# Kernel optimization log

Measured on AMD Instinct MI355X. Metric: run time of the kernel, lower is better.

The kernel has to match this reference:

```python
import jax, jax.numpy as jnp
import numpy as np

B, N, K, D, OUT = 4, 65536, 16, 8, 8
EPS = 1e-6      # BatchNorm eps from module
SLOPE = 0.2     # LeakyReLU negative slope


def setup_inputs() -> dict:
    key = jax.random.key(0)
    ks = jax.random.split(key, 4)
    coords = jax.random.normal(ks[0], (B, N, 3), jnp.float32)
    features = jax.random.normal(ks[1], (B, D, N, 1), jnp.float32)
    neighbour_indices = jax.random.randint(ks[2], (B, N, K), 0, N)
    conv_w = jax.random.normal(ks[3], (OUT, 10), jnp.float32) * 0.1  # 1x1 Conv2d weight (out,in)
    conv_b = jnp.zeros((OUT,), jnp.float32)
    bn_gamma = jnp.ones((OUT,), jnp.float32)
    bn_beta = jnp.zeros((OUT,), jnp.float32)
    return dict(coords=coords, features=features, neighbour_indices=neighbour_indices,
                conv_w=conv_w, conv_b=conv_b, bn_gamma=bn_gamma, bn_beta=bn_beta)


def _locse(coords, features, neighbour_indices, conv_w, conv_b, bn_gamma, bn_beta):
    # per-batch gather: (B,N,d),(B,N,K) -> (B,N,K,d)
    gather = jax.vmap(lambda x, i: x[i])
    nb_coords = gather(coords, neighbour_indices)                      # (B,N,K,3)
    ext = jnp.broadcast_to(coords[:, :, None, :], nb_coords.shape)     # (B,N,K,3)
    rel_pos = ext - nb_coords
    rel_dist = jnp.sqrt(jnp.sum(rel_pos * rel_pos, -1, keepdims=True))  # (B,N,K,1)
    rf = jnp.concatenate([rel_dist, rel_pos, ext, nb_coords], -1)       # (B,N,K,10)
    # SharedMLP: 1x1 conv + BatchNorm (training stats, biased var) + LeakyReLU(0.2)
    y = jnp.einsum('bnkc,oc->bnko', rf, conv_w) + conv_b                # (B,N,K,OUT)
    mean = jnp.mean(y, (0, 1, 2))
    var = jnp.mean(jnp.square(y - mean), (0, 1, 2))
    y = bn_gamma * (y - mean) * jax.lax.rsqrt(var + EPS) + bn_beta
    y = jnp.where(y >= 0, y, SLOPE * y)
    # neighbour feature gather: features (B,D,N,1) -> (B,N,D) -> (B,N,K,D)
    nf = gather(jnp.squeeze(features, -1).transpose(0, 2, 1), neighbour_indices)
    out = jnp.concatenate([nf, y], -1)                                  # (B,N,K,D+OUT)
    # match torch channel-first layout (B, 2*d, N, K)
    return jnp.moveaxis(out, -1, 1), jnp.moveaxis(y, -1, 1)


def reference(coords, features, neighbour_indices, conv_w, conv_b, bn_gamma, bn_beta):
    return _locse(coords, features, neighbour_indices, conv_w, conv_b, bn_gamma, bn_beta)
```

## Files before the change

kernel.cpp:

```cpp
#include <hip/hip_runtime.h>
#include <cstdint>
#include <cstddef>

namespace {
constexpr int Bn = 4;
constexpr int Nn = 65536;
constexpr int Kn = 16;
constexpr int NK = Nn * Kn;
constexpr int TOTAL = Bn * NK;
constexpr float COUNT_F = 4194304.0f;
constexpr float EPS = 1e-6f;
constexpr float SLOPE = 0.2f;
constexpr long long OUT0_TOTAL = (long long)Bn * 16 * NK;
}


__global__ __launch_bounds__(256) void prep_kernel(
    const float* __restrict__ coords,
    const float* __restrict__ features,
    float* __restrict__ stats,
    float4* __restrict__ cpad,
    float4* __restrict__ tf)
{
    if (blockIdx.x == 0 && threadIdx.x < 16) stats[threadIdx.x] = 0.0f;
    int t = blockIdx.x * blockDim.x + threadIdx.x;
    if (t >= Bn * Nn) return;
    int b = t >> 16;
    int n = t & (Nn - 1);
    const float* c = coords + (size_t)t * 3;
    cpad[t] = make_float4(c[0], c[1], c[2], 0.0f);
    const float* fb = features + (size_t)b * 8 * Nn + n;
    float4 lo = make_float4(fb[0 * Nn], fb[1 * Nn], fb[2 * Nn], fb[3 * Nn]);
    float4 hi = make_float4(fb[4 * Nn], fb[5 * Nn], fb[6 * Nn], fb[7 * Nn]);
    tf[2 * t]     = lo;
    tf[2 * t + 1] = hi;
}

__global__ void init_kernel(float* __restrict__ stats) {
    if (threadIdx.x < 16) stats[threadIdx.x] = 0.0f;
}

template <bool PREP>
__global__ __launch_bounds__(256) void reduce_kernel(
    const int* __restrict__ nbr,
    const float4* __restrict__ cpad,
    const float* __restrict__ coords,
    const float* __restrict__ conv_w,
    const float* __restrict__ conv_b,
    float* __restrict__ stats)
{
    float w[80];
    #pragma unroll
    for (int i = 0; i < 80; i++) w[i] = conv_w[i];
    float bb[8];
    #pragma unroll
    for (int i = 0; i < 8; i++) bb[i] = conv_b[i];

    float s[8], sq[8];
    #pragma unroll
    for (int i = 0; i < 8; i++) { s[i] = 0.0f; sq[i] = 0.0f; }

    int stride = gridDim.x * blockDim.x;
    for (int t = blockIdx.x * blockDim.x + threadIdx.x; t < TOTAL; t += stride) {
        int b = t >> 20;
        int r = t & (NK - 1);
        int n = r >> 4;
        int idx = nbr[t];
        float ex, ey, ez, nx, ny, nz;
        if (PREP) {
            float4 e = cpad[(b << 16) + n];
            float4 q = cpad[(b << 16) + idx];
            ex = e.x; ey = e.y; ez = e.z;
            nx = q.x; ny = q.y; nz = q.z;
        } else {
            const float* cb = coords + (size_t)b * Nn * 3;
            ex = cb[n * 3]; ey = cb[n * 3 + 1]; ez = cb[n * 3 + 2];
            nx = cb[idx * 3]; ny = cb[idx * 3 + 1]; nz = cb[idx * 3 + 2];
        }
        float rx = ex - nx, ry = ey - ny, rz = ez - nz;
        float dist = sqrtf(rx * rx + ry * ry + rz * rz);
        float rf[10] = {dist, rx, ry, rz, ex, ey, ez, nx, ny, nz};
        #pragma unroll
        for (int o = 0; o < 8; o++) {
            float y = bb[o];
            #pragma unroll
            for (int c = 0; c < 10; c++) y = fmaf(w[o * 10 + c], rf[c], y);
            s[o] += y;
            sq[o] = fmaf(y, y, sq[o]);
        }
    }

    #pragma unroll
    for (int i = 0; i < 8; i++) {
        #pragma unroll
        for (int off = 32; off > 0; off >>= 1) {
            s[i]  += __shfl_xor(s[i], off, 64);
            sq[i] += __shfl_xor(sq[i], off, 64);
        }
    }
    __shared__ float ls[4][16];
    int lane = threadIdx.x & 63;
    int wv = threadIdx.x >> 6;
    if (lane == 0) {
        #pragma unroll
        for (int i = 0; i < 8; i++) { ls[wv][i] = s[i]; ls[wv][8 + i] = sq[i]; }
    }
    __syncthreads();
    if (threadIdx.x < 16) {
        float a = ls[0][threadIdx.x] + ls[1][threadIdx.x]
                + ls[2][threadIdx.x] + ls[3][threadIdx.x];
        atomicAdd(&stats[threadIdx.x], a);
    }
}

__global__ void finalize_kernel(
    const float* __restrict__ conv_w,
    const float* __restrict__ conv_b,
    const float* __restrict__ gamma,
    const float* __restrict__ beta,
    float* __restrict__ stats)
{
    int j = threadIdx.x;
    if (j >= 88) return;
    int o = (j < 80) ? (j / 10) : (j - 80);
    float mean = stats[o] * (1.0f / COUNT_F);
    float var = stats[8 + o] * (1.0f / COUNT_F) - mean * mean;
    var = fmaxf(var, 0.0f);
    float scale = gamma[o] * rsqrtf(var + EPS);
    if (j < 80) stats[16 + j] = conv_w[j] * scale;
    else        stats[96 + o] = (conv_b[o] - mean) * scale + beta[o];
}

template <bool PREP>
__global__ __launch_bounds__(256) void output_kernel(
    const int* __restrict__ nbr,
    const float4* __restrict__ cpad,
    const float* __restrict__ coords,
    const float4* __restrict__ tf,
    const float* __restrict__ features,
    const float* __restrict__ stats,
    float* __restrict__ out)
{
    float w[80];
    #pragma unroll
    for (int i = 0; i < 80; i++) w[i] = stats[16 + i];
    float bb[8];
    #pragma unroll
    for (int i = 0; i < 8; i++) bb[i] = stats[96 + i];

    int stride = gridDim.x * blockDim.x;
    for (int t = blockIdx.x * blockDim.x + threadIdx.x; t < TOTAL; t += stride) {
        int b = t >> 20;
        int r = t & (NK - 1);
        int n = r >> 4;
        int idx = nbr[t];
        float ex, ey, ez, nx, ny, nz;
        if (PREP) {
            float4 e = cpad[(b << 16) + n];
            float4 q = cpad[(b << 16) + idx];
            ex = e.x; ey = e.y; ez = e.z;
            nx = q.x; ny = q.y; nz = q.z;
        } else {
            const float* cb = coords + (size_t)b * Nn * 3;
            ex = cb[n * 3]; ey = cb[n * 3 + 1]; ez = cb[n * 3 + 2];
            nx = cb[idx * 3]; ny = cb[idx * 3 + 1]; nz = cb[idx * 3 + 2];
        }
        float rx = ex - nx, ry = ey - ny, rz = ez - nz;
        float dist = sqrtf(rx * rx + ry * ry + rz * rz);
        float rf[10] = {dist, rx, ry, rz, ex, ey, ez, nx, ny, nz};

        float* o0 = out + ((size_t)b << 24) + r;
        if (PREP) {
            float4 lo = tf[2 * ((b << 16) + idx)];
            float4 hi = tf[2 * ((b << 16) + idx) + 1];
            __builtin_nontemporal_store(lo.x, o0 + 0 * (size_t)NK);
            __builtin_nontemporal_store(lo.y, o0 + 1 * (size_t)NK);
            __builtin_nontemporal_store(lo.z, o0 + 2 * (size_t)NK);
            __builtin_nontemporal_store(lo.w, o0 + 3 * (size_t)NK);
            __builtin_nontemporal_store(hi.x, o0 + 4 * (size_t)NK);
            __builtin_nontemporal_store(hi.y, o0 + 5 * (size_t)NK);
            __builtin_nontemporal_store(hi.z, o0 + 6 * (size_t)NK);
            __builtin_nontemporal_store(hi.w, o0 + 7 * (size_t)NK);
        } else {
            const float* fb = features + (size_t)b * 8 * Nn + idx;
            #pragma unroll
            for (int d = 0; d < 8; d++)
                __builtin_nontemporal_store(fb[d * Nn], o0 + (size_t)d * NK);
        }
        float* o1 = out + OUT0_TOTAL + ((size_t)(b * 8) << 20) + r;
        #pragma unroll
        for (int o = 0; o < 8; o++) {
            float y = bb[o];
            #pragma unroll
            for (int c = 0; c < 10; c++) y = fmaf(w[o * 10 + c], rf[c], y);
            float z = fmaxf(y, SLOPE * y);
            __builtin_nontemporal_store(z, o0 + (size_t)(8 + o) * NK);
            __builtin_nontemporal_store(z, o1 + (size_t)o * NK);
        }
    }
}

extern "C" void kernel_launch(void* const* d_in, const int* in_sizes, int n_in,
                              void* d_out, int out_size, void* d_ws, size_t ws_size,
                              hipStream_t stream) {
    const float* coords   = (const float*)d_in[0];
    const float* features = (const float*)d_in[1];
    const int*   nbr      = (const int*)d_in[2];
    const float* conv_w   = (const float*)d_in[3];
    const float* conv_b   = (const float*)d_in[4];
    const float* gamma    = (const float*)d_in[5];
    const float* beta     = (const float*)d_in[6];
    float* out = (float*)d_out;

    float* stats = (float*)d_ws;
    const size_t CPAD_OFF = 1024;
    const size_t CPAD_BYTES = (size_t)Bn * Nn * 4 * sizeof(float);
    const size_t TF_OFF = CPAD_OFF + CPAD_BYTES;
    const size_t TF_BYTES = (size_t)Bn * Nn * 8 * sizeof(float);
    const size_t NEED = TF_OFF + TF_BYTES;
    float4* cpad = (float4*)((char*)d_ws + CPAD_OFF);
    float4* tf   = (float4*)((char*)d_ws + TF_OFF);

    const bool prep = (ws_size >= NEED);
    if (prep) {
        prep_kernel<<<(Bn * Nn) / 256, 256, 0, stream>>>(coords, features, stats, cpad, tf);
        reduce_kernel<true><<<1024, 256, 0, stream>>>(nbr, cpad, coords, conv_w, conv_b, stats);
    } else {
        init_kernel<<<1, 64, 0, stream>>>(stats);
        reduce_kernel<false><<<1024, 256, 0, stream>>>(nbr, cpad, coords, conv_w, conv_b, stats);
    }
    finalize_kernel<<<1, 128, 0, stream>>>(conv_w, conv_b, gamma, beta, stats);
    if (prep)
        output_kernel<true><<<4096, 256, 0, stream>>>(nbr, cpad, coords, tf, features, stats, out);
    else
        output_kernel<false><<<4096, 256, 0, stream>>>(nbr, cpad, coords, tf, features, stats, out);
}
```

Baseline: 545.6 us.

## Process four neighbours per thread with vector loads/stores and XCD-aware batch mapping

Each thread now handles four consecutive neighbour slots. It loads the indices as one 128-bit nontemporal load, loads the centre coordinate once, and writes every output channel as a 128-bit nontemporal store instead of scalar stores. Blocks are mapped so that each XCD pair works on a single batch, which keeps each batch's coords and feature gather table local to one L2. The output kernel drops its grid-stride loop and assumes exactly one quad per thread for the fixed grid of 4096 blocks. This ties correctness to that launch size and raises register pressure.

```diff
diff --git a/kernel.cpp b/kernel.cpp
--- a/kernel.cpp
+++ b/kernel.cpp
@@ -1,6 +1,9 @@
 #include <hip/hip_runtime.h>
 #include <cstdint>
 #include <cstddef>
+
+typedef float v4f __attribute__((ext_vector_type(4)));
+typedef int   v4i __attribute__((ext_vector_type(4)));
 
 namespace {
 constexpr int Bn = 4;
@@ -8,6 +11,7 @@
 constexpr int Kn = 16;
 constexpr int NK = Nn * Kn;
 constexpr int TOTAL = Bn * NK;
+constexpr int QPB = NK / 4;
 constexpr float COUNT_F = 4194304.0f;
 constexpr float EPS = 1e-6f;
 constexpr float SLOPE = 0.2f;
@@ -19,8 +23,8 @@
     const float* __restrict__ coords,
     const float* __restrict__ features,
     float* __restrict__ stats,
-    float4* __restrict__ cpad,
-    float4* __restrict__ tf)
+    v4f* __restrict__ cpad,
+    v4f* __restrict__ tf)
 {
     if (blockIdx.x == 0 && threadIdx.x < 16) stats[threadIdx.x] = 0.0f;
     int t = blockIdx.x * blockDim.x + threadIdx.x;
@@ -28,10 +32,11 @@
     int b = t >> 16;
     int n = t & (Nn - 1);
     const float* c = coords + (size_t)t * 3;
-    cpad[t] = make_float4(c[0], c[1], c[2], 0.0f);
+    v4f cv = {c[0], c[1], c[2], 0.0f};
+    cpad[t] = cv;
     const float* fb = features + (size_t)b * 8 * Nn + n;
-    float4 lo = make_float4(fb[0 * Nn], fb[1 * Nn], fb[2 * Nn], fb[3 * Nn]);
-    float4 hi = make_float4(fb[4 * Nn], fb[5 * Nn], fb[6 * Nn], fb[7 * Nn]);
+    v4f lo = {fb[0 * Nn], fb[1 * Nn], fb[2 * Nn], fb[3 * Nn]};
+    v4f hi = {fb[4 * Nn], fb[5 * Nn], fb[6 * Nn], fb[7 * Nn]};
     tf[2 * t]     = lo;
     tf[2 * t + 1] = hi;
 }
@@ -42,8 +47,8 @@
 
 template <bool PREP>
 __global__ __launch_bounds__(256) void reduce_kernel(
-    const int* __restrict__ nbr,
-    const float4* __restrict__ cpad,
+    const v4i* __restrict__ nbr4,
+    const v4f* __restrict__ cpad,
     const float* __restrict__ coords,
     const float* __restrict__ conv_w,
     const float* __restrict__ conv_b,
@@ -60,33 +65,43 @@
     #pragma unroll
     for (int i = 0; i < 8; i++) { s[i] = 0.0f; sq[i] = 0.0f; }
 
-    int stride = gridDim.x * blockDim.x;
-    for (int t = blockIdx.x * blockDim.x + threadIdx.x; t < TOTAL; t += stride) {
-        int b = t >> 20;
-        int r = t & (NK - 1);
-        int n = r >> 4;
-        int idx = nbr[t];
-        float ex, ey, ez, nx, ny, nz;
+    int xcd = blockIdx.x & 7;
+    int b   = xcd >> 1;
+    int wb  = ((blockIdx.x >> 3) << 1) | (xcd & 1);
+    int stride = (gridDim.x >> 2) * blockDim.x;
+    const float* cb = coords + (size_t)b * Nn * 3;
+
+    for (int ql = wb * blockDim.x + threadIdx.x; ql < QPB; ql += stride) {
+        v4i idx = __builtin_nontemporal_load(&nbr4[(b << 18) + ql]);
+        int id[4] = {idx.x, idx.y, idx.z, idx.w};
+        int n = ql >> 2;
+        float ex, ey, ez;
         if (PREP) {
-            float4 e = cpad[(b << 16) + n];
-            float4 q = cpad[(b << 16) + idx];
+            v4f e = cpad[(b << 16) + n];
             ex = e.x; ey = e.y; ez = e.z;
-            nx = q.x; ny = q.y; nz = q.z;
         } else {
-            const float* cb = coords + (size_t)b * Nn * 3;
             ex = cb[n * 3]; ey = cb[n * 3 + 1]; ez = cb[n * 3 + 2];
-            nx = cb[idx * 3]; ny = cb[idx * 3 + 1]; nz = cb[idx * 3 + 2];
-        }
-        float rx = ex - nx, ry = ey - ny, rz = ez - nz;
-        float dist = sqrtf(rx * rx + ry * ry + rz * rz);
-        float rf[10] = {dist, rx, ry, rz, ex, ey, ez, nx, ny, nz};
-        #pragma unroll
-        for (int o = 0; o < 8; o++) {
-            float y = bb[o];
+        }
+        #pragma unroll
+        for (int k = 0; k < 4; k++) {
+            float nx, ny, nz;
+            if (PREP) {
+                v4f q = cpad[(b << 16) + id[k]];
+                nx = q.x; ny = q.y; nz = q.z;
+            } else {
+                nx = cb[id[k] * 3]; ny = cb[id[k] * 3 + 1]; nz = cb[id[k] * 3 + 2];
+            }
+            float rx = ex - nx, ry = ey - ny, rz = ez - nz;
+            float dist = sqrtf(rx * rx + ry * ry + rz * rz);
+            float rf[10] = {dist, rx, ry, rz, ex, ey, ez, nx, ny, nz};
             #pragma unroll
-            for (int c = 0; c < 10; c++) y = fmaf(w[o * 10 + c], rf[c], y);
-            s[o] += y;
-            sq[o] = fmaf(y, y, sq[o]);
+            for (int o = 0; o < 8; o++) {
+                float y = bb[o];
+                #pragma unroll
+                for (int c = 0; c < 10; c++) y = fmaf(w[o * 10 + c], rf[c], y);
+                s[o] += y;
+                sq[o] = fmaf(y, y, sq[o]);
+            }
         }
     }
 
@@ -133,10 +148,10 @@
 
 template <bool PREP>
 __global__ __launch_bounds__(256) void output_kernel(
-    const int* __restrict__ nbr,
-    const float4* __restrict__ cpad,
+    const v4i* __restrict__ nbr4,
+    const v4f* __restrict__ cpad,
     const float* __restrict__ coords,
-    const float4* __restrict__ tf,
+    const v4f* __restrict__ tf,
     const float* __restrict__ features,
     const float* __restrict__ stats,
     float* __restrict__ out)
@@ -148,55 +163,77 @@
     #pragma unroll
     for (int i = 0; i < 8; i++) bb[i] = stats[96 + i];
 
-    int stride = gridDim.x * blockDim.x;
-    for (int t = blockIdx.x * blockDim.x + threadIdx.x; t < TOTAL; t += stride) {
-        int b = t >> 20;
-        int r = t & (NK - 1);
-        int n = r >> 4;
-        int idx = nbr[t];
-        float ex, ey, ez, nx, ny, nz;
+    int xcd = blockIdx.x & 7;
+    int b   = xcd >> 1;
+    int wb  = ((blockIdx.x >> 3) << 1) | (xcd & 1);
+    int ql  = wb * blockDim.x + threadIdx.x;
+    int n   = ql >> 2;
+
+    v4i idx = __builtin_nontemporal_load(&nbr4[(b << 18) + ql]);
+    int id[4] = {idx.x, idx.y, idx.z, idx.w};
+
+    const float* cb = coords + (size_t)b * Nn * 3;
+    float ex, ey, ez;
+    if (PREP) {
+        v4f e = cpad[(b << 16) + n];
+        ex = e.x; ey = e.y; ez = e.z;
+    } else {
+        ex = cb[n * 3]; ey = cb[n * 3 + 1]; ez = cb[n * 3 + 2];
+    }
+
+    float* o0 = out + ((size_t)b << 24) + (size_t)ql * 4;
+    float* o1 = out + OUT0_TOTAL + ((size_t)(b * 8) << 20) + (size_t)ql * 4;
+
+    if (PREP) {
+        v4f lo[4], hi[4];
+        #pragma unroll
+        for (int k = 0; k < 4; k++) {
+            lo[k] = tf[2 * ((b << 16) + id[k])];
+            hi[k] = tf[2 * ((b << 16) + id[k]) + 1];
+        }
+        #pragma unroll
+        for (int c = 0; c < 4; c++) {
+            v4f vlo = {lo[0][c], lo[1][c], lo[2][c], lo[3][c]};
+            v4f vhi = {hi[0][c], hi[1][c], hi[2][c], hi[3][c]};
+            __builtin_nontemporal_store(vlo, (v4f*)(o0 + (size_t)c * NK));
+            __builtin_nontemporal_store(vhi, (v4f*)(o0 + (size_t)(4 + c) * NK));
+        }
+    } else {
+        const float* fb = features + (size_t)b * 8 * Nn;
+        #pragma unroll
+        for (int d = 0; d < 8; d++) {
+            v4f v = {fb[(size_t)d * Nn + id[0]], fb[(size_t)d * Nn + id[1]],
+                     fb[(size_t)d * Nn + id[2]], fb[(size_t)d * Nn + id[3]]};
+            __builtin_nontemporal_store(v, (v4f*)(o0 + (size_t)d * NK));
+        }
+    }
+
+    float acc[8][4];
+    #pragma unroll
+    for (int k = 0; k < 4; k++) {
+        float nx, ny, nz;
         if (PREP) {
-            float4 e = cpad[(b << 16) + n];
-            float4 q = cpad[(b << 16) + idx];
-            ex = e.x; ey = e.y; ez = e.z;
+            v4f q = cpad[(b << 16) + id[k]];
             nx = q.x; ny = q.y; nz = q.z;
         } else {
-            const float* cb = coords + (size_t)b * Nn * 3;
-            ex = cb[n * 3]; ey = cb[n * 3 + 1]; ez = cb[n * 3 + 2];
-            nx = cb[idx * 3]; ny = cb[idx * 3 + 1]; nz = cb[idx * 3 + 2];
+            nx = cb[id[k] * 3]; ny = cb[id[k] * 3 + 1]; nz = cb[id[k] * 3 + 2];
         }
         float rx = ex - nx, ry = ey - ny, rz = ez - nz;
         float dist = sqrtf(rx * rx + ry * ry + rz * rz);
         float rf[10] = {dist, rx, ry, rz, ex, ey, ez, nx, ny, nz};
-
-        float* o0 = out + ((size_t)b << 24) + r;
-        if (PREP) {
-            float4 lo = tf[2 * ((b << 16) + idx)];
-            float4 hi = tf[2 * ((b << 16) + idx) + 1];
-            __builtin_nontemporal_store(lo.x, o0 + 0 * (size_t)NK);
-            __builtin_nontemporal_store(lo.y, o0 + 1 * (size_t)NK);
-            __builtin_nontemporal_store(lo.z, o0 + 2 * (size_t)NK);
-            __builtin_nontemporal_store(lo.w, o0 + 3 * (size_t)NK);
-            __builtin_nontemporal_store(hi.x, o0 + 4 * (size_t)NK);
-            __builtin_nontemporal_store(hi.y, o0 + 5 * (size_t)NK);
-            __builtin_nontemporal_store(hi.z, o0 + 6 * (size_t)NK);
-            __builtin_nontemporal_store(hi.w, o0 + 7 * (size_t)NK);
-        } else {
-            const float* fb = features + (size_t)b * 8 * Nn + idx;
-            #pragma unroll
-            for (int d = 0; d < 8; d++)
-                __builtin_nontemporal_store(fb[d * Nn], o0 + (size_t)d * NK);
-        }
-        float* o1 = out + OUT0_TOTAL + ((size_t)(b * 8) << 20) + r;
         #pragma unroll
         for (int o = 0; o < 8; o++) {
             float y = bb[o];
             #pragma unroll
             for (int c = 0; c < 10; c++) y = fmaf(w[o * 10 + c], rf[c], y);
-            float z = fmaxf(y, SLOPE * y);
-            __builtin_nontemporal_store(z, o0 + (size_t)(8 + o) * NK);
-            __builtin_nontemporal_store(z, o1 + (size_t)o * NK);
-        }
+            acc[o][k] = fmaxf(y, SLOPE * y);
+        }
+    }
+    #pragma unroll
+    for (int o = 0; o < 8; o++) {
+        v4f v = {acc[o][0], acc[o][1], acc[o][2], acc[o][3]};
+        __builtin_nontemporal_store(v, (v4f*)(o0 + (size_t)(8 + o) * NK));
+        __builtin_nontemporal_store(v, (v4f*)(o1 + (size_t)o * NK));
     }
 }
 
@@ -211,6 +248,7 @@
     const float* gamma    = (const float*)d_in[5];
     const float* beta     = (const float*)d_in[6];
     float* out = (float*)d_out;
+    const v4i* nbr4 = (const v4i*)nbr;
 
     float* stats = (float*)d_ws;
     const size_t CPAD_OFF = 1024;
@@ -218,20 +256,20 @@
     const size_t TF_OFF = CPAD_OFF + CPAD_BYTES;
     const size_t TF_BYTES = (size_t)Bn * Nn * 8 * sizeof(float);
     const size_t NEED = TF_OFF + TF_BYTES;
-    float4* cpad = (float4*)((char*)d_ws + CPAD_OFF);
-    float4* tf   = (float4*)((char*)d_ws + TF_OFF);
+    v4f* cpad = (v4f*)((char*)d_ws + CPAD_OFF);
+    v4f* tf   = (v4f*)((char*)d_ws + TF_OFF);
 
     const bool prep = (ws_size >= NEED);
     if (prep) {
         prep_kernel<<<(Bn * Nn) / 256, 256, 0, stream>>>(coords, features, stats, cpad, tf);
-        reduce_kernel<true><<<1024, 256, 0, stream>>>(nbr, cpad, coords, conv_w, conv_b, stats);
+        reduce_kernel<true><<<1024, 256, 0, stream>>>(nbr4, cpad, coords, conv_w, conv_b, stats);
     } else {
         init_kernel<<<1, 64, 0, stream>>>(stats);
-        reduce_kernel<false><<<1024, 256, 0, stream>>>(nbr, cpad, coords, conv_w, conv_b, stats);
+        reduce_kernel<false><<<1024, 256, 0, stream>>>(nbr4, cpad, coords, conv_w, conv_b, stats);
     }
     finalize_kernel<<<1, 128, 0, stream>>>(conv_w, conv_b, gamma, beta, stats);
     if (prep)
-        output_kernel<true><<<4096, 256, 0, stream>>>(nbr, cpad, coords, tf, features, stats, out);
+        output_kernel<true><<<4096, 256, 0, stream>>>(nbr4, cpad, coords, tf, features, stats, out);
     else
-        output_kernel<false><<<4096, 256, 0, stream>>>(nbr, cpad, coords, tf, features, stats, out);
-}
+        output_kernel<false><<<4096, 256, 0, stream>>>(nbr4, cpad, coords, tf, features, stats, out);
+}
```

Result: faster. 475.0 us (-12.9%).
